# Kernel optimization log

Hardware: AMD Instinct MI355X
Metric: run time of the kernel (lower is better)

## Reference

```python
import math
import jax, jax.numpy as jnp
import numpy as np

B, T, N, F, H = 8, 16, 64, 64, 1024  # feature_dim must equal num_regions for the einsum to be valid


def _linear_init(key, out_dim, in_dim):
    kw, kb = jax.random.split(key)
    s = 1.0 / np.sqrt(in_dim)
    W = jax.random.uniform(kw, (out_dim, in_dim), jnp.float32, -s, s)
    b = jax.random.uniform(kb, (out_dim,), jnp.float32, -s, s)
    return W, b


def setup_inputs() -> dict:
    key = jax.random.key(0)
    k0, k1, k2, k3, k4 = jax.random.split(key, 5)
    M = jax.random.normal(k0, (B, T, N, N, F), jnp.float32)
    Wo, bo = _linear_init(k1, H, N * F)      # origin_proj
    Wso, bso = _linear_init(k2, N, H)        # origin_score
    Wd, bd = _linear_init(k3, H, N * F)      # dest_proj
    Wsd, bsd = _linear_init(k4, N, H)        # dest_score
    return {"M": M, "Wo": Wo, "bo": bo, "Wso": Wso, "bso": bso,
            "Wd": Wd, "bd": bd, "Wsd": Wsd, "bsd": bsd}


def _sparse_attention(scores, u):
    # scores: (BT, N, N)
    p = jax.nn.softmax(scores, axis=-1)
    entropy = -jnp.sum(p * jnp.log(p + 1e-9), axis=-1)          # (BT, N)
    _, top_idx = jax.lax.top_k(-entropy, u)                      # u smallest-entropy rows
    bt = entropy.shape[0]
    mask = jnp.zeros(entropy.shape, bool).at[jnp.arange(bt)[:, None], top_idx].set(True)
    return p * mask[..., None]                                   # zero all but u rows


def reference(M, Wo, bo, Wso, bso, Wd, bd, Wsd, bsd):
    Bb, Tt, Nn, _, Ff = M.shape
    BT = Bb * Tt
    X = M.reshape(BT, Nn, Nn * Ff)                               # origin view
    Y = jnp.transpose(M, (0, 1, 3, 2, 4)).reshape(BT, Nn, Nn * Ff)  # dest view
    omega_scores = (X @ Wo.T + bo) @ Wso.T + bso                 # (BT, N, N)
    delta_scores = (Y @ Wd.T + bd) @ Wsd.T + bsd                 # (BT, N, N)
    u = max(1, int(math.log(Nn)))
    omega = _sparse_attention(omega_scores, u)
    delta = _sparse_attention(delta_scores, u)
    M_flat = M.reshape(BT, Nn, Nn, Ff)
    out = jnp.einsum('bij,bjkl->bikl', omega, M_flat)            # (BT, N, N, F)
    out = jnp.einsum('bikl,bjl->bijk', out, delta)               # requires F == N
    return out.reshape(Bb, Tt, Nn, Nn, Ff)
```

## Files before the change

### kernel.cpp

```cpp
#include <hip/hip_runtime.h>
#include <math.h>

#define NB 8
#define NT 16
#define NN 64
#define NF 64
#define NH 1024
#define BT 128
#define NFK 4096

typedef float  f32x4 __attribute__((ext_vector_type(4)));
typedef short  s16x8 __attribute__((ext_vector_type(8)));

#define MFMA_B16(a, b, c) __builtin_amdgcn_mfma_f32_16x16x32_bf16(a, b, c, 0, 0, 0)

#define BEFF_FOFF   524288
#define PSEL_FOFF   524416
#define RTAB_FOFF   589952
#define RES_FOFF    606336
#define DYN_FOFF    868480

__device__ __forceinline__ void split_bf16(float v, unsigned short& hi, unsigned short& lo) {
    unsigned u = __float_as_uint(v);
    float r = v - __uint_as_float(u & 0xFFFF0000u);
    hi = (unsigned short)(u >> 16);
    lo = (unsigned short)(__float_as_uint(r) >> 16);
}

__device__ __forceinline__ void split8(const float4& a0, const float4& a1, s16x8& ah, s16x8& al) {
    float fa[8];
    *(float4*)&fa[0] = a0; *(float4*)&fa[4] = a1;
    #pragma unroll
    for (int j = 0; j < 8; ++j) {
        unsigned u = __float_as_uint(fa[j]);
        float r = fa[j] - __uint_as_float(u & 0xFFFF0000u);
        ah[j] = (short)(u >> 16);
        al[j] = (short)(__float_as_uint(r) >> 16);
    }
}

__global__ __launch_bounds__(256) void fold_part(
    const float* __restrict__ Wso, const float* __restrict__ Wo,
    const float* __restrict__ Wsd, const float* __restrict__ Wd,
    float* __restrict__ fpart, int hchunk)
{
    const int which = blockIdx.y, kc = blockIdx.z;
    const float* __restrict__ A  = which ? Wsd : Wso;
    const float* __restrict__ Bm = which ? Wd  : Wo;
    const int c0 = blockIdx.x * 32;

    __shared__ float As[64][68];
    __shared__ float Bs[32][68];

    const int t = threadIdx.x;
    const int tx = t & 7, ty = t >> 3;

    float acc[2][4] = {};

    const int h0beg = kc * hchunk, h0end = h0beg + hchunk;
    for (int h0 = h0beg; h0 < h0end; h0 += 64) {
        #pragma unroll
        for (int it = 0; it < 4; ++it) {
            int r = (t >> 4) + it * 16, c4 = (t & 15) * 4;
            *(float4*)&As[r][c4] = *(const float4*)&A[r * NH + h0 + c4];
        }
        #pragma unroll
        for (int it = 0; it < 2; ++it) {
            int h = (t >> 3) + it * 32, cq = t & 7;
            float4 v = *(const float4*)&Bm[(size_t)(h0 + h) * NFK + c0 + cq * 4];
            Bs[cq * 4 + 0][h] = v.x; Bs[cq * 4 + 1][h] = v.y;
            Bs[cq * 4 + 2][h] = v.z; Bs[cq * 4 + 3][h] = v.w;
        }
        __syncthreads();
        #pragma unroll 4
        for (int kk = 0; kk < 64; kk += 4) {
            float4 a4[2], b4[4];
            a4[0] = *(const float4*)&As[ty][kk];
            a4[1] = *(const float4*)&As[ty + 32][kk];
            #pragma unroll
            for (int n = 0; n < 4; ++n) b4[n] = *(const float4*)&Bs[tx + 8 * n][kk];
            #pragma unroll
            for (int m = 0; m < 2; ++m)
                #pragma unroll
                for (int n = 0; n < 4; ++n)
                    acc[m][n] += a4[m].x * b4[n].x + a4[m].y * b4[n].y
                               + a4[m].z * b4[n].z + a4[m].w * b4[n].w;
        }
        __syncthreads();
    }
    float* __restrict__ outp = fpart + ((size_t)(kc * 2 + which) * 64) * NFK;
    #pragma unroll
    for (int m = 0; m < 2; ++m)
        #pragma unroll
        for (int n = 0; n < 4; ++n)
            outp[(size_t)(ty + 32 * m) * NFK + c0 + tx + 8 * n] = acc[m][n];
}

__global__ __launch_bounds__(256) void fold_reduce(
    const float* __restrict__ fpart, unsigned short* __restrict__ wfrag, int fcc,
    const float* __restrict__ Wso, const float* __restrict__ bo, const float* __restrict__ bso,
    const float* __restrict__ Wsd, const float* __restrict__ bd, const float* __restrict__ bsd,
    float* __restrict__ beff)
{
    const int which = blockIdx.y;
    const int c0 = blockIdx.x * 64;
    const int t = threadIdx.x;
    const int r = t >> 2, cb = (t & 3) * 16;

    float s[16] = {};
    for (int c = 0; c < fcc; ++c) {
        const float* __restrict__ p =
            fpart + ((size_t)(c * 2 + which) * 64 + r) * NFK + c0 + cb;
        #pragma unroll
        for (int qq = 0; qq < 4; ++qq) {
            float4 v = *(const float4*)(p + 4 * qq);
            s[4 * qq + 0] += v.x; s[4 * qq + 1] += v.y;
            s[4 * qq + 2] += v.z; s[4 * qq + 3] += v.w;
        }
    }
    #pragma unroll
    for (int jj = 0; jj < 16; ++jj) {
        int c = c0 + cb + jj;
        unsigned short hi, lo;
        split_bf16(s[jj], hi, lo);
        int ct = r >> 4, lane = (((c >> 3) & 3) << 4) | (r & 15);
        int ks = c >> 5, j = c & 7;
        size_t offh = ((((size_t)(which * 2 + 0) * 4 + ct) * 128 + ks) * 64 + lane) * 8 + j;
        size_t offl = ((((size_t)(which * 2 + 1) * 4 + ct) * 128 + ks) * 64 + lane) * 8 + j;
        wfrag[offh] = hi;
        wfrag[offl] = lo;
    }

    if (blockIdx.x == 0) {
        const float* __restrict__ Ws = which ? Wsd : Wso;
        const float* __restrict__ bb = which ? bd  : bo;
        const float* __restrict__ bs = which ? bsd : bso;
        const int r2 = t >> 2, c2 = t & 3;
        const float* wp = Ws + r2 * NH + c2 * 256;
        const float* bp = bb + c2 * 256;
        float sacc = 0.f;
        #pragma unroll 4
        for (int i2 = 0; i2 < 64; ++i2) {
            float4 wv = *(const float4*)(wp + 4 * i2);
            float4 bv = *(const float4*)(bp + 4 * i2);
            sacc += wv.x * bv.x + wv.y * bv.y + wv.z * bv.z + wv.w * bv.w;
        }
        __shared__ float part[64][4];
        part[r2][c2] = sacc;
        __syncthreads();
        if (t < 64)
            beff[which * 64 + t] = bs[t] + part[t][0] + part[t][1] + part[t][2] + part[t][3];
    }
}

#define CHUNK(fid, ks) ((size_t)((fid) * 128 + (ks)) * 512)

__global__ __launch_bounds__(256) void scores_part(
    const float* __restrict__ M, const unsigned short* __restrict__ wfrag,
    float* __restrict__ spart, int ksc)
{
    const int bt = blockIdx.x, which = blockIdx.y, kc = blockIdx.z;
    const float* __restrict__ Mbt = M + (size_t)bt * NN * NFK;
    const int t = threadIdx.x;
    const int w = t >> 6, l = t & 63, q = l >> 4, ln = l & 15;
    const int arow = 16 * w + ln;

    __shared__ unsigned short Bsh[2][4][8][512];

    const unsigned short* __restrict__ wbase = wfrag + (size_t)which * 524288;

#define AADDR(ks) (Mbt + q * 8 + ((which == 0) \
        ? (arow * NFK + (ks) * 32) \
        : ((((ks) >> 1) * NFK) + arow * 64 + (((ks) & 1) * 32))))

    const int ks0 = kc * ksc;
    const int ngroups = ksc >> 2;

    f32x4 acc[4];
    #pragma unroll
    for (int ct = 0; ct < 4; ++ct) acc[ct] = (f32x4)0.f;

    float4 Ac[4][2], An[4][2];
    s16x8 Bn[8];

    #pragma unroll
    for (int kk = 0; kk < 4; ++kk) {
        const float* ap = AADDR(ks0 + kk);
        Ac[kk][0] = *(const float4*)ap;
        Ac[kk][1] = *(const float4*)(ap + 4);
        #pragma unroll
        for (int ii = 0; ii < 2; ++ii)
            Bn[kk * 2 + ii] = *(const s16x8*)(wbase + CHUNK(w + ii * 4, ks0 + kk) + l * 8);
    }
    #pragma unroll
    for (int kk = 0; kk < 4; ++kk)
        #pragma unroll
        for (int ii = 0; ii < 2; ++ii)
            *(s16x8*)&Bsh[0][kk][w + ii * 4][l * 8] = Bn[kk * 2 + ii];
    __syncthreads();

    int cur = 0;
    for (int g = 0; g < ngroups; ++g) {
        const bool more = (g + 1 < ngroups);
        const int ksn = ks0 + (g + 1) * 4;
        if (more) {
            #pragma unroll
            for (int kk = 0; kk < 4; ++kk) {
                const float* ap = AADDR(ksn + kk);
                An[kk][0] = *(const float4*)ap;
                An[kk][1] = *(const float4*)(ap + 4);
                #pragma unroll
                for (int ii = 0; ii < 2; ++ii)
                    Bn[kk * 2 + ii] = *(const s16x8*)(wbase + CHUNK(w + ii * 4, ksn + kk) + l * 8);
            }
        }
        #pragma unroll
        for (int kk = 0; kk < 4; ++kk) {
            s16x8 bh[4], bl[4];
            #pragma unroll
            for (int ct = 0; ct < 4; ++ct) {
                bh[ct] = *(const s16x8*)&Bsh[cur][kk][ct][l * 8];
                bl[ct] = *(const s16x8*)&Bsh[cur][kk][4 + ct][l * 8];
            }
            s16x8 ah, al;
            split8(Ac[kk][0], Ac[kk][1], ah, al);
            #pragma unroll
            for (int ct = 0; ct < 4; ++ct) {
                acc[ct] = MFMA_B16(ah, bh[ct], acc[ct]);
                acc[ct] = MFMA_B16(al, bh[ct], acc[ct]);
                acc[ct] = MFMA_B16(ah, bl[ct], acc[ct]);
            }
        }
        if (more) {
            #pragma unroll
            for (int kk = 0; kk < 4; ++kk)
                #pragma unroll
                for (int ii = 0; ii < 2; ++ii)
                    *(s16x8*)&Bsh[cur ^ 1][kk][w + ii * 4][l * 8] = Bn[kk * 2 + ii];
            #pragma unroll
            for (int kk = 0; kk < 4; ++kk) { Ac[kk][0] = An[kk][0]; Ac[kk][1] = An[kk][1]; }
            __syncthreads();
            cur ^= 1;
        }
    }
#undef AADDR

    float* __restrict__ pout = spart + ((size_t)(kc * 2 + which) * BT + bt) * 4096;
    #pragma unroll
    for (int ct = 0; ct < 4; ++ct)
        #pragma unroll
        for (int reg = 0; reg < 4; ++reg)
            pout[(16 * w + 4 * q + reg) * 64 + 16 * ct + ln] = acc[ct][reg];
}

__global__ __launch_bounds__(256) void finalize_kernel(
    const float* __restrict__ spart, const float* __restrict__ beff,
    float* __restrict__ psel, int* __restrict__ rtab, int scc)
{
    const int bt = blockIdx.x, which = blockIdx.y;
    const int t = threadIdx.x;
    const int row = t >> 2, cb = (t & 3) * 16;

    float s[16] = {};
    for (int c = 0; c < scc; ++c) {
        const float* __restrict__ p =
            spart + ((size_t)(c * 2 + which) * BT + bt) * 4096 + row * 64 + cb;
        #pragma unroll
        for (int qq = 0; qq < 4; ++qq) {
            float4 v = *(const float4*)(p + 4 * qq);
            s[4 * qq + 0] += v.x; s[4 * qq + 1] += v.y;
            s[4 * qq + 2] += v.z; s[4 * qq + 3] += v.w;
        }
    }
    #pragma unroll
    for (int jj = 0; jj < 16; ++jj) s[jj] += beff[which * 64 + cb + jj];

    float m = -INFINITY;
    #pragma unroll
    for (int jj = 0; jj < 16; ++jj) m = fmaxf(m, s[jj]);
    m = fmaxf(m, __shfl_xor(m, 1));
    m = fmaxf(m, __shfl_xor(m, 2));

    float e[16], sum = 0.f;
    #pragma unroll
    for (int jj = 0; jj < 16; ++jj) { e[jj] = expf(s[jj] - m); sum += e[jj]; }
    sum += __shfl_xor(sum, 1);
    sum += __shfl_xor(sum, 2);
    const float inv = 1.0f / sum;

    float pv[16], h = 0.f;
    #pragma unroll
    for (int jj = 0; jj < 16; ++jj) {
        pv[jj] = e[jj] * inv;
        h += pv[jj] * logf(pv[jj] + 1e-9f);
    }
    h += __shfl_xor(h, 1);
    h += __shfl_xor(h, 2);
    const float H = -h;

    __shared__ float ent[64];
    __shared__ int sel[4];
    if ((t & 3) == 0) ent[row] = H;
    __syncthreads();
    if (t == 0) {
        unsigned long long used = 0ull;
        for (int ss = 0; ss < 4; ++ss) {
            float best = INFINITY; int bi = 0;
            for (int r = 0; r < 64; ++r) {
                if ((used >> r) & 1ull) continue;
                if (ent[r] < best) { best = ent[r]; bi = r; }
            }
            used |= 1ull << bi;
            sel[ss] = bi;
        }
    }
    __syncthreads();

    int* __restrict__ rt = rtab + ((size_t)which * BT + bt) * 64;
    if (t < 64) rt[t] = -1;
    __syncthreads();
    if (t < 4) rt[sel[t]] = t;

    #pragma unroll
    for (int ss = 0; ss < 4; ++ss) {
        if (row == sel[ss]) {
            float* __restrict__ dp = psel + (((size_t)which * BT + bt) * 4 + ss) * 64 + cb;
            #pragma unroll
            for (int jj = 0; jj < 16; ++jj) dp[jj] = pv[jj];
        }
    }
}

__global__ __launch_bounds__(256) void res_compute(
    const float* __restrict__ M, const float* __restrict__ psel,
    float* __restrict__ resb2)
{
    const int bt = blockIdx.x, kc = blockIdx.y, jh = blockIdx.z;
    __shared__ float po[4][64], pd[4][64];
    __shared__ float o1[4][16][68];

    const int t = threadIdx.x;
    {
        int ss = t >> 6, ll = t & 63;
        po[ss][ll] = psel[(((size_t)0 * BT + bt) * 4 + ss) * 64 + ll];
        pd[ss][ll] = psel[(((size_t)1 * BT + bt) * 4 + ss) * 64 + ll];
    }
    __syncthreads();

    const float* __restrict__ Ms =
        M + (size_t)bt * NN * NFK + (size_t)(jh * 32) * NFK + kc * 1024 + t * 4;

    float4 a0 = {0,0,0,0}, a1 = {0,0,0,0}, a2 = {0,0,0,0}, a3 = {0,0,0,0};
    #pragma unroll 8
    for (int j = 0; j < 32; ++j) {
        float4 mv = *(const float4*)(Ms + (size_t)j * NFK);
        int jg = jh * 32 + j;
        float w0 = po[0][jg], w1 = po[1][jg], w2 = po[2][jg], w3 = po[3][jg];
        a0.x += w0 * mv.x; a0.y += w0 * mv.y; a0.z += w0 * mv.z; a0.w += w0 * mv.w;
        a1.x += w1 * mv.x; a1.y += w1 * mv.y; a1.z += w1 * mv.z; a1.w += w1 * mv.w;
        a2.x += w2 * mv.x; a2.y += w2 * mv.y; a2.z += w2 * mv.z; a2.w += w2 * mv.w;
        a3.x += w3 * mv.x; a3.y += w3 * mv.y; a3.z += w3 * mv.z; a3.w += w3 * mv.w;
    }
    {
        int kl = t >> 4, l4 = (t & 15) * 4;
        *(float4*)&o1[0][kl][l4] = a0;
        *(float4*)&o1[1][kl][l4] = a1;
        *(float4*)&o1[2][kl][l4] = a2;
        *(float4*)&o1[3][kl][l4] = a3;
    }
    __syncthreads();
    {
        int i = t >> 6, jj = (t >> 4) & 3, k = t & 15;
        float v = 0.f;
        #pragma unroll
        for (int l4 = 0; l4 < 16; ++l4) {
            float4 ov = *(const float4*)&o1[i][k][l4 * 4];
            float4 pvv = *(const float4*)&pd[jj][l4 * 4];
            v += ov.x * pvv.x + ov.y * pvv.y + ov.z * pvv.z + ov.w * pvv.w;
        }
        resb2[((((size_t)jh * BT + bt) * 4 + i) * 4 + jj) * 64 + kc * 16 + k] = v;
    }
}

__global__ __launch_bounds__(256) void writer_kernel(
    const float* __restrict__ resb2, const int* __restrict__ rtab,
    float* __restrict__ out)
{
    const int b = blockIdx.x, bt = b >> 6, i = b & 63;
    const int t = threadIdx.x;
    __shared__ float rl[4][64];
    __shared__ int jdl[64];

    const int ii = rtab[(size_t)bt * 64 + i];
    if (t < 64) jdl[t] = rtab[(size_t)BT * 64 + (size_t)bt * 64 + t];
    if (ii >= 0) {
        int jj = t >> 6, k = t & 63;
        size_t base = (((size_t)bt * 4 + ii) * 4 + jj) * 64 + k;
        rl[jj][k] = resb2[base] + resb2[(size_t)BT * 4 * 4 * 64 + base];
    }
    __syncthreads();

    float* __restrict__ dst = out + (size_t)b * 4096;
    #pragma unroll
    for (int s = 0; s < 4; ++s) {
        int p = s * 1024 + t * 4;
        int jj = p >> 6, k = p & 63;
        float4 v = {0.f, 0.f, 0.f, 0.f};
        if (ii >= 0) {
            int jd = jdl[jj];
            if (jd >= 0) v = *(const float4*)&rl[jd][k];
        }
        *(float4*)(dst + p) = v;
    }
}

extern "C" void kernel_launch(void* const* d_in, const int* in_sizes, int n_in,
                              void* d_out, int out_size, void* d_ws, size_t ws_size,
                              hipStream_t stream)
{
    const float* M   = (const float*)d_in[0];
    const float* Wo  = (const float*)d_in[1];
    const float* bo  = (const float*)d_in[2];
    const float* Wso = (const float*)d_in[3];
    const float* bso = (const float*)d_in[4];
    const float* Wd  = (const float*)d_in[5];
    const float* bd  = (const float*)d_in[6];
    const float* Wsd = (const float*)d_in[7];
    const float* bsd = (const float*)d_in[8];
    float* out = (float*)d_out;

    float* ws = (float*)d_ws;
    unsigned short* wfrag = (unsigned short*)d_ws;
    float* beff  = ws + BEFF_FOFF;
    float* psel  = ws + PSEL_FOFF;
    int*   rtab  = (int*)(ws + RTAB_FOFF);
    float* resb2 = ws + RES_FOFF;

    int FCC = 2, SCC = 4;
    {
        size_t need = ((size_t)DYN_FOFF + (size_t)FCC * 524288 + (size_t)SCC * 1048576) * 4;
        if (ws_size < need) { FCC = 1; SCC = 1; }
    }
    float* fpart = ws + DYN_FOFF;
    float* spart = fpart + (size_t)FCC * 524288;

    fold_part<<<dim3(128, 2, FCC), 256, 0, stream>>>(Wso, Wo, Wsd, Wd, fpart, NH / FCC);
    fold_reduce<<<dim3(64, 2), 256, 0, stream>>>(fpart, wfrag, FCC,
                                                 Wso, bo, bso, Wsd, bd, bsd, beff);
    scores_part<<<dim3(BT, 2, SCC), 256, 0, stream>>>(M, wfrag, spart, 128 / SCC);
    finalize_kernel<<<dim3(BT, 2), 256, 0, stream>>>(spart, beff, psel, rtab, SCC);
    res_compute<<<dim3(BT, 4, 2), 256, 0, stream>>>(M, psel, resb2);
    writer_kernel<<<BT * 64, 256, 0, stream>>>(resb2, rtab, out);
}
```

Baseline: 378.8 us.

## Shrink scores GEMM pipeline depth, split res_compute rows, raise fold split

The scores_part loop now uses a single-buffered shared-memory B tile with 2 k-steps per group instead of double-buffered 4-step groups. A register ping-pong between two A buffers replaces the copy, and an extra barrier is added per group. This cuts LDS and register use to allow more resident waves, at the cost of more synchronisation. res_compute is split into JH row chunks (default 4) for more parallel blocks, with the writer summing the JH partials, and the fold_part split factor FCC rises to 4. The workspace layout is recomputed to place the larger partial buffers.

```diff
diff --git a/kernel.cpp b/kernel.cpp
--- a/kernel.cpp
+++ b/kernel.cpp
@@ -18,7 +18,6 @@
 #define PSEL_FOFF   524416
 #define RTAB_FOFF   589952
 #define RES_FOFF    606336
-#define DYN_FOFF    868480
 
 __device__ __forceinline__ void split_bf16(float v, unsigned short& hi, unsigned short& lo) {
     unsigned u = __float_as_uint(v);
@@ -165,7 +164,7 @@
     const int w = t >> 6, l = t & 63, q = l >> 4, ln = l & 15;
     const int arow = 16 * w + ln;
 
-    __shared__ unsigned short Bsh[2][4][8][512];
+    __shared__ unsigned short Bsh[2][8][512];
 
     const unsigned short* __restrict__ wbase = wfrag + (size_t)which * 524288;
 
@@ -174,56 +173,62 @@
         : ((((ks) >> 1) * NFK) + arow * 64 + (((ks) & 1) * 32))))
 
     const int ks0 = kc * ksc;
-    const int ngroups = ksc >> 2;
+    const int ngroups = ksc >> 1;
 
     f32x4 acc[4];
     #pragma unroll
     for (int ct = 0; ct < 4; ++ct) acc[ct] = (f32x4)0.f;
 
-    float4 Ac[4][2], An[4][2];
-    s16x8 Bn[8];
-
-    #pragma unroll
-    for (int kk = 0; kk < 4; ++kk) {
-        const float* ap = AADDR(ks0 + kk);
-        Ac[kk][0] = *(const float4*)ap;
-        Ac[kk][1] = *(const float4*)(ap + 4);
-        #pragma unroll
-        for (int ii = 0; ii < 2; ++ii)
-            Bn[kk * 2 + ii] = *(const s16x8*)(wbase + CHUNK(w + ii * 4, ks0 + kk) + l * 8);
-    }
-    #pragma unroll
-    for (int kk = 0; kk < 4; ++kk)
-        #pragma unroll
-        for (int ii = 0; ii < 2; ++ii)
-            *(s16x8*)&Bsh[0][kk][w + ii * 4][l * 8] = Bn[kk * 2 + ii];
-    __syncthreads();
-
-    int cur = 0;
-    for (int g = 0; g < ngroups; ++g) {
+    float4 A0[2][2], A1[2][2];
+
+    {
+        s16x8 Bn[4];
+        #pragma unroll
+        for (int kk = 0; kk < 2; ++kk)
+            #pragma unroll
+            for (int ii = 0; ii < 2; ++ii)
+                Bn[kk * 2 + ii] = *(const s16x8*)(wbase + CHUNK(w + ii * 4, ks0 + kk) + l * 8);
+        #pragma unroll
+        for (int kk = 0; kk < 2; ++kk) {
+            const float* ap = AADDR(ks0 + kk);
+            A0[kk][0] = *(const float4*)ap;
+            A0[kk][1] = *(const float4*)(ap + 4);
+        }
+        #pragma unroll
+        for (int kk = 0; kk < 2; ++kk)
+            #pragma unroll
+            for (int ii = 0; ii < 2; ++ii)
+                *(s16x8*)&Bsh[kk][w + ii * 4][l * 8] = Bn[kk * 2 + ii];
+        __syncthreads();
+    }
+
+    auto do_group = [&](float4 (&Acur)[2][2], float4 (&Anxt)[2][2], int g) {
         const bool more = (g + 1 < ngroups);
-        const int ksn = ks0 + (g + 1) * 4;
+        const int ksn = ks0 + (g + 1) * 2;
+        s16x8 Bn[4];
         if (more) {
             #pragma unroll
-            for (int kk = 0; kk < 4; ++kk) {
-                const float* ap = AADDR(ksn + kk);
-                An[kk][0] = *(const float4*)ap;
-                An[kk][1] = *(const float4*)(ap + 4);
+            for (int kk = 0; kk < 2; ++kk)
                 #pragma unroll
                 for (int ii = 0; ii < 2; ++ii)
                     Bn[kk * 2 + ii] = *(const s16x8*)(wbase + CHUNK(w + ii * 4, ksn + kk) + l * 8);
+            #pragma unroll
+            for (int kk = 0; kk < 2; ++kk) {
+                const float* ap = AADDR(ksn + kk);
+                Anxt[kk][0] = *(const float4*)ap;
+                Anxt[kk][1] = *(const float4*)(ap + 4);
             }
         }
         #pragma unroll
-        for (int kk = 0; kk < 4; ++kk) {
+        for (int kk = 0; kk < 2; ++kk) {
             s16x8 bh[4], bl[4];
             #pragma unroll
             for (int ct = 0; ct < 4; ++ct) {
-                bh[ct] = *(const s16x8*)&Bsh[cur][kk][ct][l * 8];
-                bl[ct] = *(const s16x8*)&Bsh[cur][kk][4 + ct][l * 8];
+                bh[ct] = *(const s16x8*)&Bsh[kk][ct][l * 8];
+                bl[ct] = *(const s16x8*)&Bsh[kk][4 + ct][l * 8];
             }
             s16x8 ah, al;
-            split8(Ac[kk][0], Ac[kk][1], ah, al);
+            split8(Acur[kk][0], Acur[kk][1], ah, al);
             #pragma unroll
             for (int ct = 0; ct < 4; ++ct) {
                 acc[ct] = MFMA_B16(ah, bh[ct], acc[ct]);
@@ -231,17 +236,20 @@
                 acc[ct] = MFMA_B16(ah, bl[ct], acc[ct]);
             }
         }
+        __syncthreads();
         if (more) {
             #pragma unroll
-            for (int kk = 0; kk < 4; ++kk)
+            for (int kk = 0; kk < 2; ++kk)
                 #pragma unroll
                 for (int ii = 0; ii < 2; ++ii)
-                    *(s16x8*)&Bsh[cur ^ 1][kk][w + ii * 4][l * 8] = Bn[kk * 2 + ii];
-            #pragma unroll
-            for (int kk = 0; kk < 4; ++kk) { Ac[kk][0] = An[kk][0]; Ac[kk][1] = An[kk][1]; }
+                    *(s16x8*)&Bsh[kk][w + ii * 4][l * 8] = Bn[kk * 2 + ii];
             __syncthreads();
-            cur ^= 1;
-        }
+        }
+    };
+
+    for (int g = 0; g < ngroups; g += 2) {
+        do_group(A0, A1, g);
+        do_group(A1, A0, g + 1);
     }
 #undef AADDR
 
@@ -333,7 +341,7 @@
 
 __global__ __launch_bounds__(256) void res_compute(
     const float* __restrict__ M, const float* __restrict__ psel,
-    float* __restrict__ resb2)
+    float* __restrict__ resb2, int jrows)
 {
     const int bt = blockIdx.x, kc = blockIdx.y, jh = blockIdx.z;
     __shared__ float po[4][64], pd[4][64];
@@ -348,13 +356,13 @@
     __syncthreads();
 
     const float* __restrict__ Ms =
-        M + (size_t)bt * NN * NFK + (size_t)(jh * 32) * NFK + kc * 1024 + t * 4;
+        M + (size_t)bt * NN * NFK + (size_t)(jh * jrows) * NFK + kc * 1024 + t * 4;
 
     float4 a0 = {0,0,0,0}, a1 = {0,0,0,0}, a2 = {0,0,0,0}, a3 = {0,0,0,0};
     #pragma unroll 8
-    for (int j = 0; j < 32; ++j) {
+    for (int j = 0; j < jrows; ++j) {
         float4 mv = *(const float4*)(Ms + (size_t)j * NFK);
-        int jg = jh * 32 + j;
+        int jg = jh * jrows + j;
         float w0 = po[0][jg], w1 = po[1][jg], w2 = po[2][jg], w3 = po[3][jg];
         a0.x += w0 * mv.x; a0.y += w0 * mv.y; a0.z += w0 * mv.z; a0.w += w0 * mv.w;
         a1.x += w1 * mv.x; a1.y += w1 * mv.y; a1.z += w1 * mv.z; a1.w += w1 * mv.w;
@@ -384,7 +392,7 @@
 
 __global__ __launch_bounds__(256) void writer_kernel(
     const float* __restrict__ resb2, const int* __restrict__ rtab,
-    float* __restrict__ out)
+    float* __restrict__ out, int jh_n)
 {
     const int b = blockIdx.x, bt = b >> 6, i = b & 63;
     const int t = threadIdx.x;
@@ -396,7 +404,10 @@
     if (ii >= 0) {
         int jj = t >> 6, k = t & 63;
         size_t base = (((size_t)bt * 4 + ii) * 4 + jj) * 64 + k;
-        rl[jj][k] = resb2[base] + resb2[(size_t)BT * 4 * 4 * 64 + base];
+        float s = 0.f;
+        for (int h = 0; h < jh_n; ++h)
+            s += resb2[(size_t)h * BT * 1024 + base];
+        rl[jj][k] = s;
     }
     __syncthreads();
 
@@ -436,12 +447,16 @@
     int*   rtab  = (int*)(ws + RTAB_FOFF);
     float* resb2 = ws + RES_FOFF;
 
-    int FCC = 2, SCC = 4;
-    {
-        size_t need = ((size_t)DYN_FOFF + (size_t)FCC * 524288 + (size_t)SCC * 1048576) * 4;
-        if (ws_size < need) { FCC = 1; SCC = 1; }
-    }
-    float* fpart = ws + DYN_FOFF;
+    int FCC = 4, SCC = 4, JH = 4;
+    size_t need = ((size_t)RES_FOFF + (size_t)JH * BT * 1024
+                   + (size_t)FCC * 524288 + (size_t)SCC * 1048576) * 4;
+    if (ws_size < need) {
+        FCC = 2; SCC = 4; JH = 2;
+        need = ((size_t)RES_FOFF + (size_t)JH * BT * 1024
+                + (size_t)FCC * 524288 + (size_t)SCC * 1048576) * 4;
+        if (ws_size < need) { FCC = 1; SCC = 1; JH = 2; }
+    }
+    float* fpart = resb2 + (size_t)JH * BT * 1024;
     float* spart = fpart + (size_t)FCC * 524288;
 
     fold_part<<<dim3(128, 2, FCC), 256, 0, stream>>>(Wso, Wo, Wsd, Wd, fpart, NH / FCC);
@@ -449,6 +464,6 @@
                                                  Wso, bo, bso, Wsd, bd, bsd, beff);
     scores_part<<<dim3(BT, 2, SCC), 256, 0, stream>>>(M, wfrag, spart, 128 / SCC);
     finalize_kernel<<<dim3(BT, 2), 256, 0, stream>>>(spart, beff, psel, rtab, SCC);
-    res_compute<<<dim3(BT, 4, 2), 256, 0, stream>>>(M, psel, resb2);
-    writer_kernel<<<BT * 64, 256, 0, stream>>>(resb2, rtab, out);
-}
+    res_compute<<<dim3(BT, 4, JH), 256, 0, stream>>>(M, psel, resb2, NN / JH);
+    writer_kernel<<<BT * 64, 256, 0, stream>>>(resb2, rtab, out, JH);
+}
```

New measurement: 375.1 us. About the same (-1.0%).
